# Kernel tuning notes

Measured on AMD Instinct MI355X. Metric: run time of the kernel, lower is better.

The kernel has to match this reference:

```python
import jax, jax.numpy as jnp
import numpy as np

HIDDEN = 4096
N_HEADS = 32
N_KV_HEADS = 8
HEAD_DIM = HIDDEN // N_HEADS  # 128
GROUPS = N_HEADS // N_KV_HEADS  # 4
B, S = 1, 2048
NEG = -1e9


def setup_inputs() -> dict:
    key = jax.random.key(0)
    ks = jax.random.split(key, 8)
    hidden_states = jax.random.normal(ks[0], (B, S, HIDDEN), dtype=jnp.float32)
    # additive causal mask [B,1,S,S]
    causal = jnp.tril(jnp.ones((S, S), dtype=bool))
    attention_mask = jnp.where(causal, 0.0, NEG).astype(jnp.float32)[None, None]
    position_ids = jnp.broadcast_to(jnp.arange(S, dtype=jnp.int64), (B, S))
    inv_freq = 1.0 / (500000.0 ** (np.arange(0, HEAD_DIM, 2, dtype=np.float32) / HEAD_DIM))
    freqs = np.arange(S, dtype=np.float32)[:, None] * inv_freq[None, :]  # [S, 64]
    cos = jnp.asarray(np.cos(freqs), dtype=jnp.float32)
    sin = jnp.asarray(np.sin(freqs), dtype=jnp.float32)
    sc = 1.0 / np.sqrt(HIDDEN)
    Wq = jax.random.normal(ks[1], (HIDDEN, HIDDEN), dtype=jnp.float32) * sc
    Wk = jax.random.normal(ks[2], (N_KV_HEADS * HEAD_DIM, HIDDEN), dtype=jnp.float32) * sc
    Wv = jax.random.normal(ks[3], (N_KV_HEADS * HEAD_DIM, HIDDEN), dtype=jnp.float32) * sc
    Wo = jax.random.normal(ks[4], (HIDDEN, HIDDEN), dtype=jnp.float32) * sc
    return {"hidden_states": hidden_states, "attention_mask": attention_mask,
            "position_ids": position_ids, "cos": cos, "sin": sin,
            "Wq": Wq, "Wk": Wk, "Wv": Wv, "Wo": Wo}


def _rope(q, k, cos, sin, position_ids):
    # cos/sin: [max_pos, head_dim//2]; gather per position -> [b,1,s,hd/2]
    c = cos[position_ids][:, None]  # [b,1,s,d/2]
    s_ = sin[position_ids][:, None]
    q1, q2 = q[..., ::2], q[..., 1::2]
    k1, k2 = k[..., ::2], k[..., 1::2]
    q_rot = jnp.concatenate([q1 * c - q2 * s_, q2 * c + q1 * s_], axis=-1)
    k_rot = jnp.concatenate([k1 * c - k2 * s_, k2 * c + k1 * s_], axis=-1)
    return q_rot, k_rot


def reference(hidden_states, attention_mask, position_ids, cos, sin, Wq, Wk, Wv, Wo):
    b, s, _ = hidden_states.shape
    q = jnp.einsum('bsh,oh->bso', hidden_states, Wq).reshape(b, s, N_HEADS, HEAD_DIM).transpose(0, 2, 1, 3)
    k = jnp.einsum('bsh,oh->bso', hidden_states, Wk).reshape(b, s, N_KV_HEADS, HEAD_DIM).transpose(0, 2, 1, 3)
    v = jnp.einsum('bsh,oh->bso', hidden_states, Wv).reshape(b, s, N_KV_HEADS, HEAD_DIM).transpose(0, 2, 1, 3)
    q, k = _rope(q, k, cos, sin, position_ids)
    if GROUPS > 1:
        k = jnp.repeat(k, GROUPS, axis=1)  # [b,H,s,d]
        v = jnp.repeat(v, GROUPS, axis=1)
    scores = jnp.einsum('bhqd,bhkd->bhqk', q, k) / np.sqrt(HEAD_DIM)
    scores = scores + attention_mask
    attn = jax.nn.softmax(scores.astype(jnp.float32), axis=-1).astype(q.dtype)
    out = jnp.einsum('bhqk,bhkd->bhqd', attn, v)
    out = out.transpose(0, 2, 1, 3).reshape(b, s, HIDDEN)
    out = jnp.einsum('bso,ho->bsh', out, Wo)
    return out
```

## Files before the change

### kernel.cpp

```cpp
#include <hip/hip_runtime.h>
#include <hip/hip_bf16.h>

#define S_LEN 2048
#define HID   4096
#define NH    32
#define NKV   8
#define HD    128

typedef __attribute__((ext_vector_type(8))) short short8v;
typedef __attribute__((ext_vector_type(4))) float floatx4;

__device__ __forceinline__ float bf2f(unsigned short u) {
  union { unsigned int u32; float f; } v; v.u32 = ((unsigned int)u) << 16; return v.f;
}
__device__ __forceinline__ unsigned short f2bf(float f) {
  union { float f; unsigned int u; } v; v.f = f;
  unsigned int u = v.u + 0x7fffu + ((v.u >> 16) & 1u);
  return (unsigned short)(u >> 16);
}
__device__ __forceinline__ unsigned int cvtpk_bf16(float lo, float hi) {
  unsigned int r;
  asm("v_cvt_pk_bf16_f32 %0, %1, %2" : "=v"(r) : "v"(lo), "v"(hi));
  return r;
}

__device__ __forceinline__ void gld_lds16(const void* g, void* l) {
  __builtin_amdgcn_global_load_lds((const __attribute__((address_space(1))) void*)g,
                                   (__attribute__((address_space(3))) void*)l, 16, 0, 0);
}

__global__ __launch_bounds__(256) void cvt_all(const float* __restrict__ X,  const float* __restrict__ Wq,
                                               const float* __restrict__ Wk, const float* __restrict__ Wv,
                                               const float* __restrict__ Wo,
                                               unsigned short* __restrict__ Xb,  unsigned short* __restrict__ Wqb,
                                               unsigned short* __restrict__ Wkb, unsigned short* __restrict__ Wvb,
                                               unsigned short* __restrict__ Wob) {
  const int c0 = 2097152;
  const int c1 = c0 + 4194304;
  const int c2 = c1 + 1048576;
  const int c3 = c2 + 1048576;
  const int c4 = c3 + 4194304;
  int i = blockIdx.x * blockDim.x + threadIdx.x;
  int stride = gridDim.x * blockDim.x;
  for (; i < c4; i += stride) {
    const float* src; unsigned short* dst; int off;
    if (i < c0)      { src = X;  dst = Xb;  off = i; }
    else if (i < c1) { src = Wq; dst = Wqb; off = i - c0; }
    else if (i < c2) { src = Wk; dst = Wkb; off = i - c1; }
    else if (i < c3) { src = Wv; dst = Wvb; off = i - c2; }
    else             { src = Wo; dst = Wob; off = i - c3; }
    float4 v = ((const float4*)src)[off];
    ushort4 o;
    o.x = f2bf(v.x); o.y = f2bf(v.y); o.z = f2bf(v.z); o.w = f2bf(v.w);
    ((ushort4*)dst)[off] = o;
  }
}

__device__ __forceinline__ void gemm256_core(const unsigned short* __restrict__ A,
                                             const unsigned short* __restrict__ B,
                                             unsigned short* lds,
                                             int brow, int bcol, int tid,
                                             floatx4 acc[8][4]) {
  const int K = 4096;
  const int w = tid >> 6, lane = tid & 63;
  const int fr = lane & 15, fq = lane >> 4;
  const int wm = w >> 2, wn = w & 3;

  const int r0s = w * 32 + (lane >> 2);
  const int r1s = r0s + 16;
  const int sl0 = ((lane & 3) ^ ((r0s >> 1) & 3)) << 3;
  const int sl1 = ((lane & 3) ^ ((r1s >> 1) & 3)) << 3;
  const unsigned short* pAs0 = A + (size_t)(brow + r0s) * K + sl0;
  const unsigned short* pAs1 = A + (size_t)(brow + r1s) * K + sl1;
  const unsigned short* pBs0 = B + (size_t)(bcol + r0s) * K + sl0;
  const unsigned short* pBs1 = B + (size_t)(bcol + r1s) * K + sl1;

  const int sl = (fq ^ ((fr >> 1) & 3)) << 3;
  int aoffb[8], boffb[4];
#pragma unroll
  for (int m = 0; m < 8; ++m) aoffb[m] = (wm * 128 + m * 16 + fr) * 32 + sl;
#pragma unroll
  for (int n = 0; n < 4; ++n) boffb[n] = 16384 + (wn * 64 + n * 16 + fr) * 32 + sl;

#define STG_A(buf, kh, t)                                                     \
  do {                                                                        \
    const int ko_ = (t) * 64 + (kh) * 32;                                     \
    gld_lds16(pAs0 + ko_, lds + (buf) * 32768 + (kh) * 8192 + w * 1024);      \
    gld_lds16(pAs1 + ko_, lds + (buf) * 32768 + (kh) * 8192 + w * 1024 + 512);\
  } while (0)
#define STG_B(buf, kh, t)                                                     \
  do {                                                                        \
    const int ko_ = (t) * 64 + (kh) * 32;                                     \
    gld_lds16(pBs0 + ko_, lds + (buf) * 32768 + 16384 + (kh) * 8192 + w * 1024);      \
    gld_lds16(pBs1 + ko_, lds + (buf) * 32768 + 16384 + (kh) * 8192 + w * 1024 + 512);\
  } while (0)

  STG_A(0, 0, 0); STG_B(0, 0, 0);
  STG_A(0, 1, 0); STG_B(0, 1, 0);
  STG_A(1, 0, 1); STG_B(1, 0, 1);
  asm volatile("s_waitcnt vmcnt(8)" ::: "memory");
  __builtin_amdgcn_s_barrier();

  const int NT = K / 64;
  for (int t = 0; t < NT; ++t) {
    const int c = t & 1;
    const unsigned short* Lc = lds + c * 32768;
    short8v a_[4], b_[4], a2_[4];

#pragma unroll
    for (int m = 0; m < 4; ++m) a_[m] = *(const short8v*)&Lc[aoffb[m]];
#pragma unroll
    for (int n = 0; n < 4; ++n) b_[n] = *(const short8v*)&Lc[boffb[n]];
    if (t + 1 < NT) STG_A(c ^ 1, 1, t + 1);
    __builtin_amdgcn_s_setprio(1);
#pragma unroll
    for (int m = 0; m < 4; ++m)
#pragma unroll
      for (int n = 0; n < 4; ++n)
        acc[m][n] = __builtin_amdgcn_mfma_f32_16x16x32_bf16(a_[m], b_[n], acc[m][n], 0, 0, 0);
    __builtin_amdgcn_s_setprio(0);
    __builtin_amdgcn_s_barrier();

#pragma unroll
    for (int m = 0; m < 4; ++m) a2_[m] = *(const short8v*)&Lc[aoffb[m + 4]];
    if (t + 1 < NT) STG_B(c ^ 1, 1, t + 1);
    __builtin_amdgcn_s_setprio(1);
#pragma unroll
    for (int m = 0; m < 4; ++m)
#pragma unroll
      for (int n = 0; n < 4; ++n)
        acc[m + 4][n] = __builtin_amdgcn_mfma_f32_16x16x32_bf16(a2_[m], b_[n], acc[m + 4][n], 0, 0, 0);
    __builtin_amdgcn_s_setprio(0);
    if (t == NT - 1) asm volatile("s_waitcnt vmcnt(0)" ::: "memory");
    else             asm volatile("s_waitcnt vmcnt(8)" ::: "memory");
    __builtin_amdgcn_s_barrier();

#pragma unroll
    for (int m = 0; m < 4; ++m) a_[m] = *(const short8v*)&Lc[8192 + aoffb[m]];
#pragma unroll
    for (int n = 0; n < 4; ++n) b_[n] = *(const short8v*)&Lc[8192 + boffb[n]];
    if (t + 2 < NT) STG_A(c, 0, t + 2);
    __builtin_amdgcn_s_setprio(1);
#pragma unroll
    for (int m = 0; m < 4; ++m)
#pragma unroll
      for (int n = 0; n < 4; ++n)
        acc[m][n] = __builtin_amdgcn_mfma_f32_16x16x32_bf16(a_[m], b_[n], acc[m][n], 0, 0, 0);
    __builtin_amdgcn_s_setprio(0);
    __builtin_amdgcn_s_barrier();

#pragma unroll
    for (int m = 0; m < 4; ++m) a2_[m] = *(const short8v*)&Lc[8192 + aoffb[m + 4]];
    if (t + 2 < NT) STG_B(c, 0, t + 2);
    __builtin_amdgcn_s_setprio(1);
#pragma unroll
    for (int m = 0; m < 4; ++m)
#pragma unroll
      for (int n = 0; n < 4; ++n)
        acc[m + 4][n] = __builtin_amdgcn_mfma_f32_16x16x32_bf16(a2_[m], b_[n], acc[m + 4][n], 0, 0, 0);
    __builtin_amdgcn_s_setprio(0);
    if (t >= NT - 2) asm volatile("s_waitcnt vmcnt(0)" ::: "memory");
    else             asm volatile("s_waitcnt vmcnt(8)" ::: "memory");
    __builtin_amdgcn_s_barrier();
  }
#undef STG_A
#undef STG_B
}

__global__ __launch_bounds__(512, 2) void gemm_qkv(const unsigned short* __restrict__ Xb,
                                                   const unsigned short* __restrict__ Wqb,
                                                   const unsigned short* __restrict__ Wkb,
                                                   const unsigned short* __restrict__ Wvb,
                                                   unsigned short* __restrict__ Qg,
                                                   unsigned short* __restrict__ Kg,
                                                   unsigned short* __restrict__ Vt) {
  __shared__ unsigned short lds[2 * 32768];
  const int bx = blockIdx.x;
  const unsigned short* B; unsigned short* C; int mode, bcol, ldc;
  if (bx < 16)      { B = Wqb; C = Qg; mode = 0; bcol = bx * 256;        ldc = HID;  }
  else if (bx < 20) { B = Wkb; C = Kg; mode = 0; bcol = (bx - 16) * 256; ldc = 1024; }
  else              { B = Wvb; C = Vt; mode = 1; bcol = (bx - 20) * 256; ldc = 0;    }
  const int brow = blockIdx.y * 256;
  const int tid = threadIdx.x;
  floatx4 acc[8][4] = {};
  gemm256_core(Xb, B, lds, brow, bcol, tid, acc);

  const int w = tid >> 6, lane = tid & 63;
  const int fr = lane & 15, fq = lane >> 4;
  const int wm = w >> 2, wn = w & 3;
  const int r0 = brow + wm * 128 + fq * 4;
  const int c0 = bcol + wn * 64 + fr;
  if (mode == 0) {
#pragma unroll
    for (int m = 0; m < 8; ++m)
#pragma unroll
      for (int n = 0; n < 4; ++n)
#pragma unroll
        for (int r = 0; r < 4; ++r)
          C[(size_t)(r0 + m * 16 + r) * ldc + c0 + n * 16] = f2bf(acc[m][n][r]);
  } else {
#pragma unroll
    for (int m = 0; m < 8; ++m)
#pragma unroll
      for (int n = 0; n < 4; ++n) {
        ushort4 pk;
        pk.x = f2bf(acc[m][n][0]); pk.y = f2bf(acc[m][n][1]);
        pk.z = f2bf(acc[m][n][2]); pk.w = f2bf(acc[m][n][3]);
        *(ushort4*)&Vt[(size_t)(c0 + n * 16) * S_LEN + (r0 + m * 16)] = pk;
      }
  }
}

__global__ __launch_bounds__(512, 2) void gemm_o(const unsigned short* __restrict__ Ao,
                                                 const unsigned short* __restrict__ Wob,
                                                 float* __restrict__ Out) {
  __shared__ unsigned short lds[2 * 24576];
  const int K = 4096;
  const int tid = threadIdx.x;
  const int w = tid >> 6, lane = tid & 63;
  const int fr = lane & 15, fq = lane >> 4;
  const int wm = w >> 1, wn = w & 1;
  const int brow = blockIdx.y * 256, bcol = blockIdx.x * 128;

  const int rA = tid >> 2;
  const int sA = ((tid & 3) ^ ((rA >> 1) & 3)) << 3;
  const unsigned short* pA0 = Ao  + (size_t)(brow + rA) * K + sA;
  const unsigned short* pA1 = Ao  + (size_t)(brow + 128 + rA) * K + sA;
  const unsigned short* pB0 = Wob + (size_t)(bcol + rA) * K + sA;

  const int sl = (fq ^ ((fr >> 1) & 3)) << 3;
  int aoff[4], boff[4];
#pragma unroll
  for (int m = 0; m < 4; ++m) aoff[m] = (wm * 64 + m * 16 + fr) * 32 + sl;
#pragma unroll
  for (int n = 0; n < 4; ++n) boff[n] = 16384 + (wn * 64 + n * 16 + fr) * 32 + sl;

  floatx4 acc[4][4] = {};

#define STG_KH(buf, kh, t)                                                       \
  do {                                                                           \
    const int ko_ = (t) * 64 + (kh) * 32;                                        \
    gld_lds16(pA0 + ko_, lds + (buf) * 24576 + (kh) * 8192 + w * 512);           \
    gld_lds16(pA1 + ko_, lds + (buf) * 24576 + (kh) * 8192 + 4096 + w * 512);    \
    gld_lds16(pB0 + ko_, lds + (buf) * 24576 + 16384 + (kh) * 4096 + w * 512);   \
  } while (0)

  STG_KH(0, 0, 0);
  STG_KH(0, 1, 0);
  STG_KH(1, 0, 1);
  asm volatile("s_waitcnt vmcnt(6)" ::: "memory");
  __builtin_amdgcn_s_barrier();

  const int NT = K / 64;
  for (int t = 0; t < NT; ++t) {
    const int c = t & 1;
    const unsigned short* Lc = lds + c * 24576;
    short8v a_[4], b_[4];

#pragma unroll
    for (int m = 0; m < 4; ++m) a_[m] = *(const short8v*)&Lc[aoff[m]];
#pragma unroll
    for (int n = 0; n < 4; ++n) b_[n] = *(const short8v*)&Lc[boff[n]];
    if (t + 1 < NT) STG_KH(c ^ 1, 1, t + 1);
    __builtin_amdgcn_s_setprio(1);
#pragma unroll
    for (int m = 0; m < 4; ++m)
#pragma unroll
      for (int n = 0; n < 4; ++n)
        acc[m][n] = __builtin_amdgcn_mfma_f32_16x16x32_bf16(a_[m], b_[n], acc[m][n], 0, 0, 0);
    __builtin_amdgcn_s_setprio(0);
    if (t + 1 < NT) asm volatile("s_waitcnt vmcnt(6)" ::: "memory");
    else            asm volatile("s_waitcnt vmcnt(0)" ::: "memory");
    __builtin_amdgcn_s_barrier();

#pragma unroll
    for (int m = 0; m < 4; ++m) a_[m] = *(const short8v*)&Lc[8192 + aoff[m]];
#pragma unroll
    for (int n = 0; n < 4; ++n) b_[n] = *(const short8v*)&Lc[4096 + boff[n]];
    if (t + 2 < NT) STG_KH(c, 0, t + 2);
    __builtin_amdgcn_s_setprio(1);
#pragma unroll
    for (int m = 0; m < 4; ++m)
#pragma unroll
      for (int n = 0; n < 4; ++n)
        acc[m][n] = __builtin_amdgcn_mfma_f32_16x16x32_bf16(a_[m], b_[n], acc[m][n], 0, 0, 0);
    __builtin_amdgcn_s_setprio(0);
    if (t + 2 < NT)      asm volatile("s_waitcnt vmcnt(6)" ::: "memory");
    else if (t + 1 < NT) asm volatile("s_waitcnt vmcnt(3)" ::: "memory");
    else                 asm volatile("s_waitcnt vmcnt(0)" ::: "memory");
    __builtin_amdgcn_s_barrier();
  }
#undef STG_KH

  const int r0 = brow + wm * 64 + fq * 4;
  const int c0 = bcol + wn * 64 + fr;
#pragma unroll
  for (int m = 0; m < 4; ++m)
#pragma unroll
    for (int n = 0; n < 4; ++n)
#pragma unroll
      for (int r = 0; r < 4; ++r)
        Out[(size_t)(r0 + m * 16 + r) * HID + c0 + n * 16] = acc[m][n][r];
}

__global__ __launch_bounds__(256) void rope_kernel(const unsigned short* __restrict__ In,
                                                   const float* __restrict__ cosT,
                                                   const float* __restrict__ sinT,
                                                   unsigned short* __restrict__ Out,
                                                   int nh, float scale) {
  int idx = blockIdx.x * 256 + threadIdx.x;
  int j = idx & 63;
  int s = (idx >> 6) & (S_LEN - 1);
  int h = idx >> 17;
  unsigned int pr = *(const unsigned int*)(In + (size_t)s * (nh * HD) + h * HD + 2 * j);
  float q1 = bf2f((unsigned short)(pr & 0xffffu));
  float q2 = bf2f((unsigned short)(pr >> 16));
  float c = cosT[s * 64 + j], sn = sinT[s * 64 + j];
  unsigned short* op = Out + ((size_t)h * S_LEN + s) * HD + j;
  op[0]  = f2bf(scale * (q1 * c - q2 * sn));
  op[64] = f2bf(scale * (q2 * c + q1 * sn));
}

__global__ __launch_bounds__(256) void attn_fwd(const unsigned short* __restrict__ Qr,
                                                const unsigned short* __restrict__ Kr,
                                                const unsigned short* __restrict__ Vt,
                                                unsigned short* __restrict__ Ao) {
  __shared__ unsigned short Kl[2][64 * 128];
  __shared__ unsigned short Vl[2][64 * 128];
  const int id = blockIdx.x;
  const int swz = (id & 7) * 128 + (id >> 3);
  const int h  = swz >> 5;
  const int qt = 31 - (swz & 31);
  const int hk = h >> 2;
  const int qb = qt * 64;
  const int tid = threadIdx.x, w = tid >> 6, lane = tid & 63;
  const int fr = lane & 15, fq = lane >> 4;

  short8v aq[4];
  {
    const unsigned short* qp = Qr + ((size_t)(h * S_LEN + qb + w * 16 + fr)) * HD + fq * 8;
#pragma unroll
    for (int ks = 0; ks < 4; ++ks) aq[ks] = *(const short8v*)(qp + ks * 32);
  }

  const int kcb = ((tid & 15) * 16) ^ (((tid >> 4) & 7) << 4);
  const unsigned short* pK0 = Kr + ((size_t)hk * S_LEN + (tid >> 4)) * HD + (kcb >> 1);
  const int vcb = ((tid & 7) * 16) ^ (((tid >> 3) & 7) << 4);
  const unsigned short* pV0 = Vt + ((size_t)hk * HD + (tid >> 3)) * S_LEN + (vcb >> 1);

  const int hsel = fq >> 1;
  const int srcA = fr + ((2 * (fq & 1)) << 4);
  const int srcB = fr + ((2 * (fq & 1) + 1) << 4);

  float l_acc = 0.f;
  floatx4 o[8] = {};

#define STAGE(buf, t)                                                          \
  do {                                                                         \
    const unsigned short* pk_ = pK0 + (size_t)(t) * 64 * HD;                   \
    const unsigned short* pv_ = pV0 + (t) * 64;                                \
    _Pragma("unroll")                                                          \
    for (int j = 0; j < 4; ++j)                                                \
      gld_lds16(pk_ + (size_t)j * 16 * HD, &Kl[buf][w * 512 + j * 2048]);      \
    _Pragma("unroll")                                                          \
    for (int j = 0; j < 4; ++j)                                                \
      gld_lds16(pv_ + (size_t)j * 32 * S_LEN, &Vl[buf][w * 512 + j * 2048]);   \
  } while (0)

  STAGE(0, 0);
  asm volatile("s_waitcnt vmcnt(0)" ::: "memory");
  __syncthreads();

  int cur = 0;
  for (int t = 0; t <= qt; ++t) {
    const int kv0 = t * 64;
    if (t < qt) STAGE(cur ^ 1, t + 1);

    floatx4 St[4] = {};
    const unsigned short* Kc = &Kl[cur][0];
    const unsigned short* Vc = &Vl[cur][0];
    __builtin_amdgcn_s_setprio(1);
#pragma unroll
    for (int ks = 0; ks < 4; ++ks) {
#pragma unroll
      for (int n = 0; n < 4; ++n) {
        int row = n * 16 + fr;
        int cb = (ks * 64 + fq * 16) ^ ((row & 7) << 4);
        short8v kf = *(const short8v*)&Kc[row * 128 + (cb >> 1)];
        St[n] = __builtin_amdgcn_mfma_f32_16x16x32_bf16(kf, aq[ks], St[n], 0, 0, 0);
      }
    }
    __builtin_amdgcn_s_setprio(0);

    if (t == qt) {
#pragma unroll
      for (int n = 0; n < 4; ++n) {
#pragma unroll
        for (int r = 0; r < 4; ++r) {
          int kvg = kv0 + n * 16 + fq * 4 + r;
          if (kvg > qb + w * 16 + fr) St[n][r] = -1e30f;
        }
      }
    }

    unsigned int pk[4][2];
#pragma unroll
    for (int n = 0; n < 4; ++n) {
      float p0 = exp2f(St[n][0]);
      float p1 = exp2f(St[n][1]);
      float p2 = exp2f(St[n][2]);
      float p3 = exp2f(St[n][3]);
      l_acc += (p0 + p1) + (p2 + p3);
      pk[n][0] = cvtpk_bf16(p0, p1);
      pk[n][1] = cvtpk_bf16(p2, p3);
    }

    short8v pa[2];
#pragma unroll
    for (int ks = 0; ks < 2; ++ks) {
      unsigned int v0a = __shfl(pk[2 * ks][0], srcA), v0b = __shfl(pk[2 * ks + 1][0], srcA);
      unsigned int v1a = __shfl(pk[2 * ks][1], srcA), v1b = __shfl(pk[2 * ks + 1][1], srcA);
      unsigned int v2a = __shfl(pk[2 * ks][0], srcB), v2b = __shfl(pk[2 * ks + 1][0], srcB);
      unsigned int v3a = __shfl(pk[2 * ks][1], srcB), v3b = __shfl(pk[2 * ks + 1][1], srcB);
      uint4 u;
      u.x = hsel ? v0b : v0a;
      u.y = hsel ? v1b : v1a;
      u.z = hsel ? v2b : v2a;
      u.w = hsel ? v3b : v3a;
      pa[ks] = *(short8v*)&u;
    }

    __builtin_amdgcn_s_setprio(1);
#pragma unroll
    for (int nf = 0; nf < 8; ++nf) {
#pragma unroll
      for (int ks = 0; ks < 2; ++ks) {
        int row = nf * 16 + fr;
        int cb = (ks * 64 + fq * 16) ^ ((row & 7) << 4);
        short8v bv = *(const short8v*)&Vc[row * 64 + (cb >> 1)];
        o[nf] = __builtin_amdgcn_mfma_f32_16x16x32_bf16(pa[ks], bv, o[nf], 0, 0, 0);
      }
    }
    __builtin_amdgcn_s_setprio(0);

    if (t < qt) {
      asm volatile("s_waitcnt vmcnt(0)" ::: "memory");
      __syncthreads();
      cur ^= 1;
    }
  }
#undef STAGE

  float L = l_acc;
  L += __shfl_xor(L, 16);
  L += __shfl_xor(L, 32);
  float rinv[4];
#pragma unroll
  for (int r = 0; r < 4; ++r) rinv[r] = 1.0f / __shfl(L, fq * 4 + r);

  unsigned short* aop = Ao + (size_t)(qb + w * 16 + fq * 4) * HID + h * HD + fr;
#pragma unroll
  for (int nf = 0; nf < 8; ++nf)
#pragma unroll
    for (int r = 0; r < 4; ++r)
      aop[(size_t)r * HID + nf * 16] = f2bf(o[nf][r] * rinv[r]);
}

extern "C" void kernel_launch(void* const* d_in, const int* in_sizes, int n_in,
                              void* d_out, int out_size, void* d_ws, size_t ws_size,
                              hipStream_t stream) {
  (void)in_sizes; (void)n_in; (void)out_size; (void)ws_size;
  const float* X    = (const float*)d_in[0];
  const float* cosT = (const float*)d_in[3];
  const float* sinT = (const float*)d_in[4];
  const float* Wq   = (const float*)d_in[5];
  const float* Wk   = (const float*)d_in[6];
  const float* Wv   = (const float*)d_in[7];
  const float* Wo   = (const float*)d_in[8];

  char* ws = (char*)d_ws;
  size_t off = 0;
  auto alloc = [&](size_t bytes) { char* p = ws + off; off += (bytes + 255) & ~(size_t)255; return p; };
  unsigned short* Xb  = (unsigned short*)alloc((size_t)S_LEN * HID * 2);
  unsigned short* Wqb = (unsigned short*)alloc((size_t)HID * HID * 2);
  unsigned short* Wkb = (unsigned short*)alloc((size_t)1024 * HID * 2);
  unsigned short* Wvb = (unsigned short*)alloc((size_t)1024 * HID * 2);
  unsigned short* Wob = (unsigned short*)alloc((size_t)HID * HID * 2);
  unsigned short* Qg  = (unsigned short*)alloc((size_t)S_LEN * HID * 2);
  unsigned short* Kg  = (unsigned short*)alloc((size_t)S_LEN * 1024 * 2);
  unsigned short* Vt  = (unsigned short*)alloc((size_t)1024 * S_LEN * 2);
  unsigned short* Qr = Wqb;
  unsigned short* Kr = Wqb + (size_t)NH * S_LEN * HD;
  unsigned short* Ao = Xb;

  cvt_all<<<2048, 256, 0, stream>>>(X, Wq, Wk, Wv, Wo, Xb, Wqb, Wkb, Wvb, Wob);
  gemm_qkv<<<dim3(24, 8), 512, 0, stream>>>(Xb, Wqb, Wkb, Wvb, Qg, Kg, Vt);
  rope_kernel<<<(NH * S_LEN * 64) / 256, 256, 0, stream>>>(Qg, cosT, sinT, Qr, NH, 0.12751744f);
  rope_kernel<<<(NKV * S_LEN * 64) / 256, 256, 0, stream>>>(Kg, cosT, sinT, Kr, NKV, 1.0f);
  attn_fwd<<<1024, 256, 0, stream>>>(Qr, Kr, Vt, Ao);
  gemm_o<<<dim3(32, 8), 512, 0, stream>>>(Ao, Wob, (float*)d_out);
}
```

Before: 323.0 us.

## Fuse Q RoPE into attention load, interleave K RoPE layout, add GEMM fences

Drops the separate Q RoPE kernel: attention now reads raw Q straight from the projection output and applies the rotation and softmax scale in registers while loading its Q fragments. K RoPE now writes interleaved pairs (a permutation of head_dim, consistent for Q and K) with packed 32-bit stores. The main GEMM loop also gains an extra barrier plus an lgkmcnt(0) wait and scheduling fence before each MFMA block. These remove a kernel launch and a full write and reread of Q, at the cost of extra synchronisation in the GEMM and a little extra per-block work in attention.

```diff
diff --git a/kernel.cpp b/kernel.cpp
--- a/kernel.cpp
+++ b/kernel.cpp
@@ -95,6 +95,10 @@
     gld_lds16(pBs1 + ko_, lds + (buf) * 32768 + 16384 + (kh) * 8192 + w * 1024 + 512);\
   } while (0)
 
+#define LGKM0_FENCE                                                \
+  asm volatile("s_waitcnt lgkmcnt(0)" ::: "memory");               \
+  __builtin_amdgcn_sched_barrier(0)
+
   STG_A(0, 0, 0); STG_B(0, 0, 0);
   STG_A(0, 1, 0); STG_B(0, 1, 0);
   STG_A(1, 0, 1); STG_B(1, 0, 1);
@@ -112,6 +116,8 @@
 #pragma unroll
     for (int n = 0; n < 4; ++n) b_[n] = *(const short8v*)&Lc[boffb[n]];
     if (t + 1 < NT) STG_A(c ^ 1, 1, t + 1);
+    __builtin_amdgcn_s_barrier();
+    LGKM0_FENCE;
     __builtin_amdgcn_s_setprio(1);
 #pragma unroll
     for (int m = 0; m < 4; ++m)
@@ -124,6 +130,8 @@
 #pragma unroll
     for (int m = 0; m < 4; ++m) a2_[m] = *(const short8v*)&Lc[aoffb[m + 4]];
     if (t + 1 < NT) STG_B(c ^ 1, 1, t + 1);
+    __builtin_amdgcn_s_barrier();
+    LGKM0_FENCE;
     __builtin_amdgcn_s_setprio(1);
 #pragma unroll
     for (int m = 0; m < 4; ++m)
@@ -140,6 +148,8 @@
 #pragma unroll
     for (int n = 0; n < 4; ++n) b_[n] = *(const short8v*)&Lc[8192 + boffb[n]];
     if (t + 2 < NT) STG_A(c, 0, t + 2);
+    __builtin_amdgcn_s_barrier();
+    LGKM0_FENCE;
     __builtin_amdgcn_s_setprio(1);
 #pragma unroll
     for (int m = 0; m < 4; ++m)
@@ -152,6 +162,8 @@
 #pragma unroll
     for (int m = 0; m < 4; ++m) a2_[m] = *(const short8v*)&Lc[8192 + aoffb[m + 4]];
     if (t + 2 < NT) STG_B(c, 0, t + 2);
+    __builtin_amdgcn_s_barrier();
+    LGKM0_FENCE;
     __builtin_amdgcn_s_setprio(1);
 #pragma unroll
     for (int m = 0; m < 4; ++m)
@@ -165,6 +177,7 @@
   }
 #undef STG_A
 #undef STG_B
+#undef LGKM0_FENCE
 }
 
 __global__ __launch_bounds__(512, 2) void gemm_qkv(const unsigned short* __restrict__ Xb,
@@ -303,25 +316,26 @@
         Out[(size_t)(r0 + m * 16 + r) * HID + c0 + n * 16] = acc[m][n][r];
 }
 
-__global__ __launch_bounds__(256) void rope_kernel(const unsigned short* __restrict__ In,
-                                                   const float* __restrict__ cosT,
-                                                   const float* __restrict__ sinT,
-                                                   unsigned short* __restrict__ Out,
-                                                   int nh, float scale) {
+__global__ __launch_bounds__(256) void rope_k(const unsigned short* __restrict__ In,
+                                              const float* __restrict__ cosT,
+                                              const float* __restrict__ sinT,
+                                              unsigned short* __restrict__ Out) {
   int idx = blockIdx.x * 256 + threadIdx.x;
   int j = idx & 63;
   int s = (idx >> 6) & (S_LEN - 1);
   int h = idx >> 17;
-  unsigned int pr = *(const unsigned int*)(In + (size_t)s * (nh * HD) + h * HD + 2 * j);
-  float q1 = bf2f((unsigned short)(pr & 0xffffu));
-  float q2 = bf2f((unsigned short)(pr >> 16));
+  unsigned int pr = *(const unsigned int*)(In + (size_t)s * (NKV * HD) + h * HD + 2 * j);
+  float k1 = bf2f((unsigned short)(pr & 0xffffu));
+  float k2 = bf2f((unsigned short)(pr >> 16));
   float c = cosT[s * 64 + j], sn = sinT[s * 64 + j];
-  unsigned short* op = Out + ((size_t)h * S_LEN + s) * HD + j;
-  op[0]  = f2bf(scale * (q1 * c - q2 * sn));
-  op[64] = f2bf(scale * (q2 * c + q1 * sn));
-}
-
-__global__ __launch_bounds__(256) void attn_fwd(const unsigned short* __restrict__ Qr,
+  unsigned int pk = (unsigned int)f2bf(k1 * c - k2 * sn) |
+                    ((unsigned int)f2bf(k2 * c + k1 * sn) << 16);
+  *(unsigned int*)(Out + ((size_t)h * S_LEN + s) * HD + 2 * j) = pk;
+}
+
+__global__ __launch_bounds__(256) void attn_fwd(const unsigned short* __restrict__ Qg,
+                                                const float* __restrict__ cosT,
+                                                const float* __restrict__ sinT,
                                                 const unsigned short* __restrict__ Kr,
                                                 const unsigned short* __restrict__ Vt,
                                                 unsigned short* __restrict__ Ao) {
@@ -338,9 +352,26 @@
 
   short8v aq[4];
   {
-    const unsigned short* qp = Qr + ((size_t)(h * S_LEN + qb + w * 16 + fr)) * HD + fq * 8;
-#pragma unroll
-    for (int ks = 0; ks < 4; ++ks) aq[ks] = *(const short8v*)(qp + ks * 32);
+    const int s_row = qb + w * 16 + fr;
+    const unsigned short* qp = Qg + (size_t)s_row * HID + h * HD + fq * 8;
+    const float* cb = cosT + s_row * 64;
+    const float* sb = sinT + s_row * 64;
+    const float SC = 0.12751744f;
+#pragma unroll
+    for (int ks = 0; ks < 4; ++ks) {
+      short8v raw = *(const short8v*)(qp + ks * 32);
+      short8v ov;
+#pragma unroll
+      for (int e = 0; e < 4; ++e) {
+        float q1 = bf2f((unsigned short)raw[2 * e]);
+        float q2 = bf2f((unsigned short)raw[2 * e + 1]);
+        int j = ks * 16 + fq * 4 + e;
+        float c = cb[j], sn = sb[j];
+        ov[2 * e]     = (short)f2bf(SC * (q1 * c - q2 * sn));
+        ov[2 * e + 1] = (short)f2bf(SC * (q2 * c + q1 * sn));
+      }
+      aq[ks] = ov;
+    }
   }
 
   const int kcb = ((tid & 15) * 16) ^ (((tid >> 4) & 7) << 4);
@@ -489,14 +520,12 @@
   unsigned short* Qg  = (unsigned short*)alloc((size_t)S_LEN * HID * 2);
   unsigned short* Kg  = (unsigned short*)alloc((size_t)S_LEN * 1024 * 2);
   unsigned short* Vt  = (unsigned short*)alloc((size_t)1024 * S_LEN * 2);
-  unsigned short* Qr = Wqb;
-  unsigned short* Kr = Wqb + (size_t)NH * S_LEN * HD;
+  unsigned short* Kr = Wqb;
   unsigned short* Ao = Xb;
 
   cvt_all<<<2048, 256, 0, stream>>>(X, Wq, Wk, Wv, Wo, Xb, Wqb, Wkb, Wvb, Wob);
   gemm_qkv<<<dim3(24, 8), 512, 0, stream>>>(Xb, Wqb, Wkb, Wvb, Qg, Kg, Vt);
-  rope_kernel<<<(NH * S_LEN * 64) / 256, 256, 0, stream>>>(Qg, cosT, sinT, Qr, NH, 0.12751744f);
-  rope_kernel<<<(NKV * S_LEN * 64) / 256, 256, 0, stream>>>(Kg, cosT, sinT, Kr, NKV, 1.0f);
-  attn_fwd<<<1024, 256, 0, stream>>>(Qr, Kr, Vt, Ao);
+  rope_k<<<(NKV * S_LEN * 64) / 256, 256, 0, stream>>>(Kg, cosT, sinT, Kr);
+  attn_fwd<<<1024, 256, 0, stream>>>(Qg, cosT, sinT, Kr, Vt, Ao);
   gemm_o<<<dim3(32, 8), 512, 0, stream>>>(Ao, Wob, (float*)d_out);
 }
```

Result: no change. 324.2 us (+0.4%).
